# Optimization experiments

Hardware: AMD Instinct MI355X
Metric: run time of the kernel (lower is better)

## Reference

```python
import jax, jax.numpy as jnp
import numpy as np

B, S, D, H = 4, 2048, 1024, 16
HD = D // H  # head_dim = 64


def setup_inputs() -> dict:
    key = jax.random.key(0)
    k1, k2, k3 = jax.random.split(key, 3)
    x = jax.random.normal(k1, (B, S, D), dtype=jnp.float32)
    W_attn = jax.random.normal(k2, (D, 3 * D), dtype=jnp.float32) * (1.0 / np.sqrt(D))
    b_attn = jnp.zeros((3 * D,), dtype=jnp.float32)
    W_proj = jax.random.normal(k3, (D, D), dtype=jnp.float32) * (1.0 / np.sqrt(D))
    b_proj = jnp.zeros((D,), dtype=jnp.float32)
    return {"x": x, "W_attn": W_attn, "b_attn": b_attn, "W_proj": W_proj, "b_proj": b_proj}


def reference(x, W_attn, b_attn, W_proj, b_proj):
    bsz, seq_len, d = x.shape
    n_head = H
    head_dim = d // n_head
    qkv = x @ W_attn + b_attn                      # [B,S,3D]
    q, k, v = jnp.split(qkv, 3, axis=-1)           # each [B,S,D]
    # -> [B,H,S,hd]
    q = q.reshape(bsz, seq_len, n_head, head_dim).transpose(0, 2, 1, 3)
    k = k.reshape(bsz, seq_len, n_head, head_dim).transpose(0, 2, 1, 3)
    v = v.reshape(bsz, seq_len, n_head, head_dim).transpose(0, 2, 1, 3)
    scale = 1.0 / np.sqrt(head_dim).astype(np.float32)
    att = jnp.einsum("bhqd,bhkd->bhqk", q, k) * scale  # [B,H,S,S]
    causal = jnp.tril(jnp.ones((seq_len, seq_len), dtype=bool))
    att = jnp.where(causal[None, None], att, jnp.float32(-jnp.inf))
    att = jax.nn.softmax(att, axis=-1)
    y = jnp.einsum("bhqk,bhkd->bhqd", att, v)       # [B,H,S,hd]
    y = y.transpose(0, 2, 1, 3).reshape(bsz, seq_len, d)
    return y @ W_proj + b_proj
```

## Files before the change

### kernel.cpp

```cpp
#include <hip/hip_runtime.h>

typedef __attribute__((ext_vector_type(8))) short short8;
typedef __attribute__((ext_vector_type(8))) __bf16 bf16x8;
typedef __attribute__((ext_vector_type(2))) __bf16 bf16x2;
typedef __attribute__((ext_vector_type(4))) float f32x4;
typedef __attribute__((ext_vector_type(2))) unsigned int uint2v;

#define LOG2E 1.44269504088896340736f

__device__ __forceinline__ unsigned short f2b(float f) {
  unsigned u = __builtin_bit_cast(unsigned, f);
  u += 0x7fffu + ((u >> 16) & 1u);
  return (unsigned short)(u >> 16);
}
__device__ __forceinline__ float b2f(unsigned short s) {
  unsigned u = (unsigned)s << 16;
  return __builtin_bit_cast(float, u);
}
__device__ __forceinline__ bf16x8 asbf(short8 s) { return __builtin_bit_cast(bf16x8, s); }

__device__ __forceinline__ void gl_lds16(const void* g, void* l) {
  __builtin_amdgcn_global_load_lds(
      (const __attribute__((address_space(1))) void*)g,
      (__attribute__((address_space(3))) void*)l, 16, 0, 0);
}

__device__ __forceinline__ unsigned lds_a(const void* p) {
  return (unsigned)(size_t)(__attribute__((address_space(3))) const void*)p;
}

__device__ __forceinline__ unsigned pk_bf16(float a, float b) {
  bf16x2 v;
  v[0] = (__bf16)a;
  v[1] = (__bf16)b;
  return __builtin_bit_cast(unsigned, v);
}

template <int N>
__device__ __forceinline__ void wait_vm() {
  if constexpr (N == 7) asm volatile("s_waitcnt vmcnt(7)" ::: "memory");
  else if constexpr (N == 6) asm volatile("s_waitcnt vmcnt(6)" ::: "memory");
  else if constexpr (N == 5) asm volatile("s_waitcnt vmcnt(5)" ::: "memory");
  else if constexpr (N == 4) asm volatile("s_waitcnt vmcnt(4)" ::: "memory");
  else if constexpr (N == 2) asm volatile("s_waitcnt vmcnt(2)" ::: "memory");
  else asm volatile("s_waitcnt vmcnt(0)" ::: "memory");
}

__global__ void k_cvt_bf16(const float* __restrict__ x, unsigned short* __restrict__ o, int n) {
  int i = (blockIdx.x * 256 + threadIdx.x) * 4;
  if (i >= n) return;
  float4 v = *(const float4*)(x + i);
  ushort4 r;
  r.x = f2b(v.x); r.y = f2b(v.y); r.z = f2b(v.z); r.w = f2b(v.w);
  *(ushort4*)(o + i) = r;
}

__global__ void k_transpose_bf16(const float* __restrict__ W, unsigned short* __restrict__ Wt,
                                 int R, int C) {
  __shared__ float tile[64][65];
  const int tc = blockIdx.x, tr = blockIdx.y;
  const int r0 = tr * 64, c0 = tc * 64;
  for (int it = 0; it < 16; ++it) {
    int lin = it * 256 + threadIdx.x;
    int r = lin >> 6, c = lin & 63;
    tile[r][c] = W[(size_t)(r0 + r) * C + c0 + c];
  }
  __syncthreads();
  for (int it = 0; it < 16; ++it) {
    int lin = it * 256 + threadIdx.x;
    int orr = lin >> 6, oc = lin & 63;
    Wt[(size_t)(c0 + orr) * R + r0 + oc] = f2b(tile[oc][orr]);
  }
}

template <int BNW, bool OUT_BF16>
__global__ __launch_bounds__(512)
void k_gemm256(const unsigned short* __restrict__ A, const unsigned short* __restrict__ Bt,
               const float* __restrict__ bias, void* __restrict__ Cp,
               int M, int N, int K) {
  constexpr int BN = BNW * 4;
  constexpr int NR = BNW / 16;
  __shared__ unsigned short lds[2][(256 + BN) * 64];

  const int tid = threadIdx.x;
  const int wv = tid >> 6, lane = tid & 63;
  const int g = lane >> 4, l15 = lane & 15;
  const int wr = wv >> 2, wc = wv & 3;

  const int ntn = N / BN;
  const int nwg = gridDim.x;
  const int bid = blockIdx.x;
  const int cpx = nwg >> 3;
  const int swz = (bid & 7) * cpx + (bid >> 3);
  const int tm = swz / ntn, tn = swz % ntn;

  const unsigned short* Ab = A + (size_t)(tm * 256) * K;
  const unsigned short* Bb = Bt + (size_t)(tn * BN) * K;

  const int NT = K >> 6, NI = NT >> 1;

  auto As = [&](int buf) -> char* { return (char*)&lds[buf][0]; };
  auto Bs = [&](int buf) -> char* { return (char*)&lds[buf][256 * 64]; };

  auto stageB = [&](int buf, int t) {
#pragma unroll
    for (int it = 0; it < NR; ++it) {
      int cidx = it * 8 + wv;
      int row = cidx * 8 + (lane >> 3);
      int sc = (lane & 7) ^ (row & 7);
      gl_lds16(Bb + (size_t)row * K + t * 64 + sc * 8, Bs(buf) + cidx * 1024 + lane * 16);
    }
  };
  auto stageA = [&](int buf, int t, int q) {
    int row0 = (wv < 4) ? (q * 32 + wv * 8) : (128 + q * 32 + (wv - 4) * 8);
    int row = row0 + (lane >> 3);
    int sc = (lane & 7) ^ (row & 7);
    gl_lds16(Ab + (size_t)row * K + t * 64 + sc * 8, As(buf) + row0 * 128 + lane * 16);
  };

  auto rdA = [&](int buf, int q, int ms, int kh) -> short8 {
    int row = wr * 128 + q * 32 + ms * 16 + l15;
    int ch = (kh * 4 + g) ^ (row & 7);
    return *(const short8*)(As(buf) + row * 128 + ch * 16);
  };
  auto rdB = [&](int buf, int n, int kh) -> short8 {
    int row = wc * BNW + n * 16 + l15;
    int ch = (kh * 4 + g) ^ (row & 7);
    return *(const short8*)(Bs(buf) + row * 128 + ch * 16);
  };

  f32x4 acc[8][NR] = {};
  short8 bfr[NR][2];

  stageB(0, 0);
#pragma unroll
  for (int q = 0; q < 4; ++q) stageA(0, 0, q);
  stageB(1, 1);
#pragma unroll
  for (int q = 0; q < 3; ++q) stageA(1, 1, q);
  wait_vm<NR + 3>();
  __builtin_amdgcn_s_barrier();

  for (int i = 0; i < NI; ++i) {
    const int t0 = 2 * i;
#pragma unroll
    for (int half = 0; half < 2; ++half) {
#pragma unroll
      for (int q = 0; q < 4; ++q) {
        short8 afr[2][2];
#pragma unroll
        for (int ms = 0; ms < 2; ++ms)
#pragma unroll
          for (int kh = 0; kh < 2; ++kh) afr[ms][kh] = rdA(half, q, ms, kh);
        if (q == 0) {
#pragma unroll
          for (int n = 0; n < NR; ++n)
#pragma unroll
            for (int kh = 0; kh < 2; ++kh) bfr[n][kh] = rdB(half, n, kh);
        }
        if (half == 0) {
          if (q == 0) stageA(1, t0 + 1, 3);
          if (q == 1 && t0 + 2 < NT) { stageB(0, t0 + 2); stageA(0, t0 + 2, 0); }
          if (q == 2 && t0 + 2 < NT) stageA(0, t0 + 2, 1);
          if (q == 3 && t0 + 2 < NT) stageA(0, t0 + 2, 2);
        } else {
          if (q == 0 && t0 + 2 < NT) stageA(0, t0 + 2, 3);
          if (q == 1 && t0 + 3 < NT) stageB(1, t0 + 3);
          if (q == 2 && t0 + 3 < NT) stageA(1, t0 + 3, 0);
          if (q == 3 && t0 + 3 < NT) { stageA(1, t0 + 3, 1); stageA(1, t0 + 3, 2); }
        }
        __builtin_amdgcn_s_barrier();
        asm volatile("s_waitcnt lgkmcnt(0)" ::: "memory");
        __builtin_amdgcn_sched_barrier(0);
        __builtin_amdgcn_s_setprio(1);
#pragma unroll
        for (int n = 0; n < NR; ++n)
#pragma unroll
          for (int ms = 0; ms < 2; ++ms)
#pragma unroll
            for (int kh = 0; kh < 2; ++kh)
              acc[q * 2 + ms][n] = __builtin_amdgcn_mfma_f32_16x16x32_bf16(
                  asbf(afr[ms][kh]), asbf(bfr[n][kh]), acc[q * 2 + ms][n], 0, 0, 0);
        __builtin_amdgcn_s_setprio(0);
        if (q == 3) {
          const bool more = (half == 0) ? (t0 + 2 < NT) : (t0 + 3 < NT);
          if (more) wait_vm<NR + 3>();
          else      wait_vm<0>();
        }
        __builtin_amdgcn_s_barrier();
      }
    }
  }

  const int crow0 = tm * 256 + wr * 128 + g * 4;
  const int ccol0 = tn * BN + wc * BNW + l15;
#pragma unroll
  for (int n = 0; n < NR; ++n) {
    int col = ccol0 + n * 16;
    float bv = bias[col];
#pragma unroll
    for (int mq = 0; mq < 8; ++mq)
#pragma unroll
      for (int j = 0; j < 4; ++j) {
        int row = crow0 + mq * 16 + j;
        float v = acc[mq][n][j] + bv;
        if constexpr (OUT_BF16)
          ((unsigned short*)Cp)[(size_t)row * N + col] = f2b(v);
        else
          ((float*)Cp)[(size_t)row * N + col] = v;
      }
  }
}

__global__ __launch_bounds__(512)
void k_attn(const unsigned short* __restrict__ qkv, unsigned short* __restrict__ y) {
  constexpr int SEQ = 2048, TD = 3072, DM = 1024;
  __shared__ unsigned short Kl[3][4096];
  __shared__ unsigned short Vl[3][4096];
  __shared__ unsigned short Pl[8][2048];

  const int f = blockIdx.x;
  const int wrk = (f & 7) * 32 + (f >> 3);
  const int bh = wrk >> 2, pr = wrk & 3;
  const int b = bh >> 4, h = bh & 15;
  const int tid = threadIdx.x;
  const int lane = tid & 63, w = tid >> 6;
  const int g = lane >> 4, l15 = lane & 15;

  const size_t base = (size_t)b * SEQ * TD + h * 64;
  const unsigned short* Kg0 = qkv + base + 1024;
  const unsigned short* Vg0 = qkv + base + 2048;

  short8 onesb;
#pragma unroll
  for (int i = 0; i < 8; ++i) onesb[i] = (short)0x3F80;

  auto stage = [&](int buf, int c) {
    const unsigned short* Kg = Kg0 + (size_t)(c * 64) * TD;
    const unsigned short* Vg = Vg0 + (size_t)(c * 64) * TD;
    const int j = tid;
    int r = j >> 3, cc = j & 7;
    int cck = cc ^ (r & 7);
    gl_lds16(Kg + (size_t)r * TD + cck * 8, (char*)Kl[buf] + j * 16);
    int kv = ((j >> 1) & 3) | (((j >> 5) & 1) << 2) | (((j >> 3) & 3) << 3) |
             (((j >> 6) & 1) << 5);
    int d0 = ((j >> 7) << 4) | ((j & 1) << 3);
    gl_lds16(Vg + (size_t)kv * TD + d0, (char*)Vl[buf] + j * 16);
  };

  char* pw = (char*)Pl + w * 4096;

  for (int half = 0; half < 2; ++half) {
    const int qt = half ? (7 - pr) : pr;
    const int q0 = qt * 256;
    const int qw = w * 32;

    short8 qf[2][2];
#pragma unroll
    for (int qg = 0; qg < 2; ++qg) {
      const unsigned short* qrow = qkv + base + (size_t)(q0 + qw + qg * 16 + l15) * TD;
#pragma unroll
      for (int kh = 0; kh < 2; ++kh) {
        short8 t = *(const short8*)(qrow + kh * 32 + g * 8);
#pragma unroll
        for (int i = 0; i < 8; ++i)
          t[i] = (short)f2b(b2f((unsigned short)t[i]) * (0.125f * LOG2E));
        qf[qg][kh] = t;
      }
    }

    f32x4 o[2][4] = {};
    f32x4 ol[2] = {};

    const int nch = 4 * (qt + 1);
    stage(0, 0);
    stage(1, 1);
    int cur = 0;
    for (int c = 0; c < nch; ++c) {
      if (c + 1 < nch) wait_vm<2>();
      else             wait_vm<0>();
      __builtin_amdgcn_s_barrier();
      if (c + 2 < nch) {
        int nb = cur + 2;
        if (nb >= 3) nb -= 3;
        stage(nb, c + 2);
      }

      f32x4 sv[2][4];
      __builtin_amdgcn_s_setprio(1);
#pragma unroll
      for (int ff = 0; ff < 4; ++ff) {
        int kv = ff * 16 + l15;
        short8 kf0 = *(const short8*)((const char*)Kl[cur] + kv * 128 + ((g) ^ (kv & 7)) * 16);
        short8 kf1 = *(const short8*)((const char*)Kl[cur] + kv * 128 + ((4 + g) ^ (kv & 7)) * 16);
#pragma unroll
        for (int qg = 0; qg < 2; ++qg) {
          f32x4 s = {};
          s = __builtin_amdgcn_mfma_f32_16x16x32_bf16(asbf(kf0), asbf(qf[qg][0]), s, 0, 0, 0);
          s = __builtin_amdgcn_mfma_f32_16x16x32_bf16(asbf(kf1), asbf(qf[qg][1]), s, 0, 0, 0);
          sv[qg][ff] = s;
        }
      }
      __builtin_amdgcn_s_setprio(0);

      const int crel = c - 4 * qt;
      if (crel >= 0) {
#pragma unroll
        for (int qg = 0; qg < 2; ++qg)
#pragma unroll
          for (int ff = 0; ff < 4; ++ff)
#pragma unroll
            for (int r = 0; r < 4; ++r)
              if (crel * 64 + ff * 16 + g * 4 + r > qw + qg * 16 + l15)
                sv[qg][ff][r] = -128.f;
      }

#pragma unroll
      for (int qg = 0; qg < 2; ++qg)
#pragma unroll
        for (int ff = 0; ff < 4; ++ff) {
          float p0 = __builtin_amdgcn_exp2f(sv[qg][ff][0]);
          float p1 = __builtin_amdgcn_exp2f(sv[qg][ff][1]);
          float p2 = __builtin_amdgcn_exp2f(sv[qg][ff][2]);
          float p3 = __builtin_amdgcn_exp2f(sv[qg][ff][3]);
          unsigned w0 = pk_bf16(p0, p1);
          unsigned w1 = pk_bf16(p2, p3);
          unsigned long long pk = (unsigned long long)w0 | ((unsigned long long)w1 << 32);
          int off = qg * 2048 + ((l15 * 128 + ff * 32 + g * 8) ^ ((l15 & 7) << 4));
          *(unsigned long long*)(pw + off) = pk;
        }

      const unsigned vaddr = lds_a((const char*)Vl[cur] + g * 128 + l15 * 8);
#pragma unroll
      for (int kvh = 0; kvh < 2; ++kvh) {
        uint2v t0[4], t1[4];
#pragma unroll
        for (int n = 0; n < 4; ++n) {
          asm volatile("ds_read_b64_tr_b16 %0, %1 offset:%2"
                       : "=v"(t0[n]) : "v"(vaddr), "i"(n * 2048 + kvh * 1024));
          asm volatile("ds_read_b64_tr_b16 %0, %1 offset:%2"
                       : "=v"(t1[n]) : "v"(vaddr), "i"(n * 2048 + kvh * 1024 + 512));
        }
        asm volatile("s_waitcnt lgkmcnt(0)" ::: "memory");
        __builtin_amdgcn_sched_barrier(0);
        __builtin_amdgcn_s_setprio(1);
#pragma unroll
        for (int qg = 0; qg < 2; ++qg) {
          short8 pa = *(const short8*)(pw + qg * 2048 +
                                       ((l15 * 128 + kvh * 64 + g * 16) ^ ((l15 & 7) << 4)));
#pragma unroll
          for (int n = 0; n < 4; ++n) {
            union { uint2v u[2]; short8 s; } uu;
            uu.u[0] = t0[n]; uu.u[1] = t1[n];
            o[qg][n] = __builtin_amdgcn_mfma_f32_16x16x32_bf16(asbf(pa), asbf(uu.s),
                                                               o[qg][n], 0, 0, 0);
          }
          ol[qg] = __builtin_amdgcn_mfma_f32_16x16x32_bf16(asbf(pa), asbf(onesb),
                                                           ol[qg], 0, 0, 0);
        }
        __builtin_amdgcn_s_setprio(0);
      }

      ++cur;
      if (cur >= 3) cur -= 3;
    }

    __builtin_amdgcn_s_barrier();

#pragma unroll
    for (int qg = 0; qg < 2; ++qg) {
      float lj[4];
#pragma unroll
      for (int j = 0; j < 4; ++j) lj[j] = 1.f / ol[qg][j];
#pragma unroll
      for (int n = 0; n < 4; ++n)
#pragma unroll
        for (int j = 0; j < 4; ++j) {
          int row = q0 + qw + qg * 16 + g * 4 + j;
          int col = h * 64 + n * 16 + l15;
          y[(size_t)(b * SEQ + row) * DM + col] = f2b(o[qg][n][j] * lj[j]);
        }
    }
  }
}

extern "C" void kernel_launch(void* const* d_in, const int* in_sizes, int n_in,
                              void* d_out, int out_size, void* d_ws, size_t ws_size,
                              hipStream_t stream) {
  const float* x = (const float*)d_in[0];
  const float* W_attn = (const float*)d_in[1];
  const float* b_attn = (const float*)d_in[2];
  const float* W_proj = (const float*)d_in[3];
  const float* b_proj = (const float*)d_in[4];
  float* out = (float*)d_out;

  const int B = 4, S = 2048, D = 1024;
  const int M = B * S;
  const int TD = 3 * D;

  char* ws = (char*)d_ws;
  unsigned short* qkvb = (unsigned short*)ws;
  unsigned short* xb = (unsigned short*)(ws + (size_t)M * TD * 2);
  unsigned short* Wat = (unsigned short*)(ws + (size_t)M * TD * 2 + (size_t)M * D * 2);
  unsigned short* Wpt = Wat + (size_t)TD * D;

  k_cvt_bf16<<<(M * D) / 1024, 256, 0, stream>>>(x, xb, M * D);
  k_transpose_bf16<<<dim3(TD / 64, D / 64), 256, 0, stream>>>(W_attn, Wat, D, TD);
  k_transpose_bf16<<<dim3(D / 64, D / 64), 256, 0, stream>>>(W_proj, Wpt, D, D);

  k_gemm256<48, true><<<(M / 256) * (TD / 192), 512, 0, stream>>>(xb, Wat, b_attn, qkvb, M, TD, D);
  k_attn<<<256, 512, 0, stream>>>(qkvb, xb);
  k_gemm256<32, false><<<(M / 256) * (D / 128), 512, 0, stream>>>(xb, Wpt, b_proj, out, M, D, D);
}
```

Baseline: 165.1 us.

## Replace QKV GEMM with BK=32, 256x128 tile double-buffered kernel

Adds a new GEMM kernel for the QKV projection that uses a K-step of 32 instead of 64, a 256x128 output tile instead of 256x192, and split A/B staging interleaved between MFMA phases with two barriers per iteration. The smaller LDS footprint and the larger grid are meant to raise occupancy and wave count across CUs, and the finer-grained staging is meant to overlap global loads with compute. In exchange it runs more loop iterations and barriers per tile, and it writes the output with scalar stores that may coalesce poorly.

```diff
diff --git a/kernel.cpp b/kernel.cpp
--- a/kernel.cpp
+++ b/kernel.cpp
@@ -43,6 +43,7 @@
   else if constexpr (N == 5) asm volatile("s_waitcnt vmcnt(5)" ::: "memory");
   else if constexpr (N == 4) asm volatile("s_waitcnt vmcnt(4)" ::: "memory");
   else if constexpr (N == 2) asm volatile("s_waitcnt vmcnt(2)" ::: "memory");
+  else if constexpr (N == 1) asm volatile("s_waitcnt vmcnt(1)" ::: "memory");
   else asm volatile("s_waitcnt vmcnt(0)" ::: "memory");
 }
 
@@ -70,6 +71,137 @@
     int lin = it * 256 + threadIdx.x;
     int orr = lin >> 6, oc = lin & 63;
     Wt[(size_t)(c0 + orr) * R + r0 + oc] = f2b(tile[oc][orr]);
+  }
+}
+
+__global__ __launch_bounds__(512)
+void k_gemm_bk32(const unsigned short* __restrict__ A, const unsigned short* __restrict__ Bt,
+                 const float* __restrict__ bias, unsigned short* __restrict__ Cp,
+                 int M, int N, int K) {
+  constexpr int BNW = 32, NR = 2, BN = 128;
+  __shared__ unsigned short lds[2][384 * 32];
+
+  const int tid = threadIdx.x;
+  const int lane = tid & 63;
+  const int wv = tid >> 6;
+  const int g = lane >> 4, l15 = lane & 15;
+  const int wr = wv >> 2, wc = wv & 3;
+
+  const int ntn = N / BN;
+  const int nwg = gridDim.x;
+  const int bid = blockIdx.x;
+  const int cpx = nwg >> 3;
+  const int swz = (bid & 7) * cpx + (bid >> 3);
+  const int tm = swz / ntn, tn = swz % ntn;
+
+  const unsigned short* Ab = A + (size_t)(tm * 256) * K;
+  const unsigned short* Bb = Bt + (size_t)(tn * BN) * K;
+
+  const int NT = K >> 5;
+
+  auto As = [&](int buf) -> char* { return (char*)&lds[buf][0]; };
+  auto Bs = [&](int buf) -> char* { return (char*)&lds[buf][256 * 32]; };
+
+  auto stageA = [&](int buf, int t) {
+#pragma unroll
+    for (int it = 0; it < 2; ++it) {
+      int cidx = it * 512 + tid;
+      int row = cidx >> 2, c8 = cidx & 3;
+      int sc = c8 ^ ((row >> 1) & 3);
+      gl_lds16(Ab + (size_t)row * K + t * 32 + sc * 8, As(buf) + cidx * 16);
+    }
+  };
+  auto stageB = [&](int buf, int t) {
+    int cidx = tid;
+    int row = cidx >> 2, c8 = cidx & 3;
+    int sc = c8 ^ ((row >> 1) & 3);
+    gl_lds16(Bb + (size_t)row * K + t * 32 + sc * 8, Bs(buf) + cidx * 16);
+  };
+
+  auto rdA = [&](int buf, int ms) -> short8 {
+    int row = wr * 128 + ms * 16 + l15;
+    int ch = g ^ ((row >> 1) & 3);
+    return *(const short8*)(As(buf) + row * 64 + ch * 16);
+  };
+  auto rdB = [&](int buf, int n) -> short8 {
+    int row = wc * BNW + n * 16 + l15;
+    int ch = g ^ ((row >> 1) & 3);
+    return *(const short8*)(Bs(buf) + row * 64 + ch * 16);
+  };
+
+  f32x4 acc[8][NR] = {};
+
+  stageA(0, 0);
+  stageB(0, 0);
+  stageB(1, 1);
+  wait_vm<1>();
+  __builtin_amdgcn_s_barrier();
+
+  for (int t = 0; t < NT; ++t) {
+    const int buf = t & 1, nbuf = buf ^ 1;
+    short8 bfr[NR], a0, a1;
+
+    if (t + 1 < NT) stageA(nbuf, t + 1);
+#pragma unroll
+    for (int n = 0; n < NR; ++n) bfr[n] = rdB(buf, n);
+    a0 = rdA(buf, 0);
+    a1 = rdA(buf, 1);
+    asm volatile("s_waitcnt lgkmcnt(0)" ::: "memory");
+    __builtin_amdgcn_sched_barrier(0);
+    __builtin_amdgcn_s_barrier();
+    __builtin_amdgcn_s_setprio(1);
+#pragma unroll
+    for (int n = 0; n < NR; ++n) {
+      acc[0][n] = __builtin_amdgcn_mfma_f32_16x16x32_bf16(asbf(a0), asbf(bfr[n]), acc[0][n], 0, 0, 0);
+      acc[1][n] = __builtin_amdgcn_mfma_f32_16x16x32_bf16(asbf(a1), asbf(bfr[n]), acc[1][n], 0, 0, 0);
+    }
+    a0 = rdA(buf, 2);
+    a1 = rdA(buf, 3);
+#pragma unroll
+    for (int n = 0; n < NR; ++n) {
+      acc[2][n] = __builtin_amdgcn_mfma_f32_16x16x32_bf16(asbf(a0), asbf(bfr[n]), acc[2][n], 0, 0, 0);
+      acc[3][n] = __builtin_amdgcn_mfma_f32_16x16x32_bf16(asbf(a1), asbf(bfr[n]), acc[3][n], 0, 0, 0);
+    }
+    __builtin_amdgcn_s_setprio(0);
+
+    if (t + 2 < NT) stageB(buf, t + 2);
+    a0 = rdA(buf, 4);
+    a1 = rdA(buf, 5);
+    asm volatile("s_waitcnt lgkmcnt(0)" ::: "memory");
+    __builtin_amdgcn_sched_barrier(0);
+    __builtin_amdgcn_s_barrier();
+    __builtin_amdgcn_s_setprio(1);
+#pragma unroll
+    for (int n = 0; n < NR; ++n) {
+      acc[4][n] = __builtin_amdgcn_mfma_f32_16x16x32_bf16(asbf(a0), asbf(bfr[n]), acc[4][n], 0, 0, 0);
+      acc[5][n] = __builtin_amdgcn_mfma_f32_16x16x32_bf16(asbf(a1), asbf(bfr[n]), acc[5][n], 0, 0, 0);
+    }
+    a0 = rdA(buf, 6);
+    a1 = rdA(buf, 7);
+#pragma unroll
+    for (int n = 0; n < NR; ++n) {
+      acc[6][n] = __builtin_amdgcn_mfma_f32_16x16x32_bf16(asbf(a0), asbf(bfr[n]), acc[6][n], 0, 0, 0);
+      acc[7][n] = __builtin_amdgcn_mfma_f32_16x16x32_bf16(asbf(a1), asbf(bfr[n]), acc[7][n], 0, 0, 0);
+    }
+    __builtin_amdgcn_s_setprio(0);
+    if (t + 2 < NT) wait_vm<1>();
+    else            wait_vm<0>();
+    __builtin_amdgcn_s_barrier();
+  }
+
+  const int crow0 = tm * 256 + wr * 128 + g * 4;
+  const int ccol0 = tn * BN + wc * BNW + l15;
+#pragma unroll
+  for (int n = 0; n < NR; ++n) {
+    int col = ccol0 + n * 16;
+    float bv = bias[col];
+#pragma unroll
+    for (int mq = 0; mq < 8; ++mq)
+#pragma unroll
+      for (int j = 0; j < 4; ++j) {
+        int row = crow0 + mq * 16 + j;
+        Cp[(size_t)row * N + col] = f2b(acc[mq][n][j] + bv);
+      }
   }
 }
 
@@ -408,7 +540,7 @@
   k_transpose_bf16<<<dim3(TD / 64, D / 64), 256, 0, stream>>>(W_attn, Wat, D, TD);
   k_transpose_bf16<<<dim3(D / 64, D / 64), 256, 0, stream>>>(W_proj, Wpt, D, D);
 
-  k_gemm256<48, true><<<(M / 256) * (TD / 192), 512, 0, stream>>>(xb, Wat, b_attn, qkvb, M, TD, D);
+  k_gemm_bk32<<<(M / 256) * (TD / 128), 512, 0, stream>>>(xb, Wat, b_attn, qkvb, M, TD, D);
   k_attn<<<256, 512, 0, stream>>>(qkvb, xb);
   k_gemm256<32, false><<<(M / 256) * (D / 128), 512, 0, stream>>>(xb, Wpt, b_proj, out, M, D, D);
 }
```

Result: no change. 164.9 us (-0.1%).
